# Kernel optimization log

Hardware: AMD Instinct MI355X
Metric: run time of the kernel (lower is better)

## Reference

```python
import jax, jax.numpy as jnp
import numpy as np

I = 16    # nutrition_input_size
H = 128   # hidden_size
B = 64
S = 4096
MLP = 64


def setup_inputs() -> dict:
    key = jax.random.key(0)
    ks = jax.random.split(key, 16)
    sc = 0.05
    inp = {
        "nutrition_data": jax.random.normal(ks[0], (B, S, I), dtype=jnp.float32),
        # GRU layer 0 (input size I)
        "w_ih0": sc * jax.random.normal(ks[1], (3 * H, I), dtype=jnp.float32),
        "w_hh0": sc * jax.random.normal(ks[2], (3 * H, H), dtype=jnp.float32),
        "b_ih0": sc * jax.random.normal(ks[3], (3 * H,), dtype=jnp.float32),
        "b_hh0": sc * jax.random.normal(ks[4], (3 * H,), dtype=jnp.float32),
        # GRU layer 1 (input size H)
        "w_ih1": sc * jax.random.normal(ks[5], (3 * H, H), dtype=jnp.float32),
        "w_hh1": sc * jax.random.normal(ks[6], (3 * H, H), dtype=jnp.float32),
        "b_ih1": sc * jax.random.normal(ks[7], (3 * H,), dtype=jnp.float32),
        "b_hh1": sc * jax.random.normal(ks[8], (3 * H,), dtype=jnp.float32),
        # metabolism increment head: Linear(H+I, 64) -> ReLU -> Linear(64, 1)
        "w1": sc * jax.random.normal(ks[9], (MLP, H + I), dtype=jnp.float32),
        "b1": sc * jax.random.normal(ks[10], (MLP,), dtype=jnp.float32),
        "w2": sc * jax.random.normal(ks[11], (1, MLP), dtype=jnp.float32),
        "b2": sc * jax.random.normal(ks[12], (1,), dtype=jnp.float32),
        "initial_metabolism": jnp.float32(2.5),
    }
    return inp


def _gru_layer(x, w_ih, w_hh, b_ih, b_hh):
    # x: [B, S, D]; PyTorch GRU cell math, gate order (r, z, n).
    gi = jnp.einsum("bsd,gd->bsg", x, w_ih) + b_ih  # [B, S, 3H]
    h0 = jnp.zeros((x.shape[0], w_hh.shape[1]), dtype=x.dtype)

    def step(h, gi_t):
        gh = h @ w_hh.T + b_hh  # [B, 3H]
        i_r, i_z, i_n = jnp.split(gi_t, 3, axis=-1)
        h_r, h_z, h_n = jnp.split(gh, 3, axis=-1)
        r = jax.nn.sigmoid(i_r + h_r)
        z = jax.nn.sigmoid(i_z + h_z)
        n = jnp.tanh(i_n + r * h_n)
        h_new = (1.0 - z) * n + z * h
        return h_new, h_new

    _, hs = jax.lax.scan(step, h0, jnp.swapaxes(gi, 0, 1))  # hs: [S, B, H]
    return jnp.swapaxes(hs, 0, 1)  # [B, S, H]


def reference(nutrition_data, w_ih0, w_hh0, b_ih0, b_hh0,
              w_ih1, w_hh1, b_ih1, b_hh1,
              w1, b1, w2, b2, initial_metabolism):
    # 2-layer GRU (dropout is inactive in eval; identical math without it)
    h1 = _gru_layer(nutrition_data, w_ih0, w_hh0, b_ih0, b_hh0)
    gru_out = _gru_layer(h1, w_ih1, w_hh1, b_ih1, b_hh1)  # [B, S, H]

    # Per-timestep head is independent of recurrence: batch it over all t,
    # then replace the sequential additive accumulation with a cumsum.
    combined = jnp.concatenate([gru_out, nutrition_data], axis=-1)  # [B, S, H+I]
    hdn = jax.nn.relu(jnp.einsum("bsf,mf->bsm", combined, w1) + b1)
    inc = jnp.tanh(jnp.einsum("bsm,om->bso", hdn, w2) + b2) * 0.125  # [B, S, 1]
    out = initial_metabolism + jnp.cumsum(inc, axis=1)  # [B, S, 1]
    return out
```

## Files before the change

kernel.cpp:

```cpp
#include <hip/hip_runtime.h>
#include <cmath>

#define B 64
#define S 4096
#define NI 16
#define H 128
#define F 144
#define CH 16
#define NCH (S / CH)
#define GIP 201

typedef _Float16 h2   __attribute__((ext_vector_type(2)));
typedef _Float16 h8   __attribute__((ext_vector_type(8)));
typedef float    f4v  __attribute__((ext_vector_type(4)));
typedef unsigned long long u64;
typedef u64 u64x2 __attribute__((ext_vector_type(2)));

__device__ __forceinline__ float rcp_fast(float x) { return __builtin_amdgcn_rcpf(x); }
__device__ __forceinline__ float sigf(float x) {
    return rcp_fast(1.0f + __expf(-x));
}
__device__ __forceinline__ float tanh_fast(float x) {
    const float e = __expf(-2.0f * x);
    return fmaf(2.0f, rcp_fast(1.0f + e), -1.0f);
}
__device__ __forceinline__ float pair_reduce(float v) {
    int t1 = __builtin_amdgcn_mov_dpp(__float_as_int(v), 0xB1, 0xf, 0xf, true);
    v += __int_as_float(t1);
    return v;
}
__device__ __forceinline__ h2 cvt2(float a, float b) {
    h2 r; r[0] = (_Float16)a; r[1] = (_Float16)b; return r;
}
__device__ __forceinline__ void cvt8(const float* p, h2* w) {
    const float4 f0 = ((const float4*)p)[0];
    const float4 f1 = ((const float4*)p)[1];
    w[0] = cvt2(f0.x, f0.y); w[1] = cvt2(f0.z, f0.w);
    w[2] = cvt2(f1.x, f1.y); w[3] = cvt2(f1.z, f1.w);
}
__device__ __forceinline__ h8 cvt8v(const float* p) {
    const float4 f0 = ((const float4*)p)[0];
    const float4 f1 = ((const float4*)p)[1];
    h8 r;
    r[0] = (_Float16)f0.x; r[1] = (_Float16)f0.y;
    r[2] = (_Float16)f0.z; r[3] = (_Float16)f0.w;
    r[4] = (_Float16)f1.x; r[5] = (_Float16)f1.y;
    r[6] = (_Float16)f1.z; r[7] = (_Float16)f1.w;
    return r;
}
__device__ __forceinline__ void pin_h2(h2& v) {
    int t = __builtin_bit_cast(int, v);
    asm volatile("" : "+v"(t));
    v = __builtin_bit_cast(h2, t);
}
__device__ __forceinline__ void pin_f(float& v) {
    asm volatile("" : "+v"(v));
}
__device__ __forceinline__ void pin_h8(h8& v) {
    u64x2 t = __builtin_bit_cast(u64x2, v);
    u64 a = t[0], b = t[1];
    asm volatile("" : "+v"(a), "+v"(b));
    t[0] = a; t[1] = b;
    v = __builtin_bit_cast(h8, t);
}
__device__ __forceinline__ f4v mfma16(h8 a, h8 b, f4v c) {
    return __builtin_amdgcn_mfma_f32_16x16x32_f16(a, b, c, 0, 0, 0);
}

__device__ __forceinline__ void store_y0(void* p, uint2 v) {
    __hip_atomic_store((u64*)p, __builtin_bit_cast(u64, v),
                       __ATOMIC_RELAXED, __HIP_MEMORY_SCOPE_AGENT);
}
__device__ __forceinline__ h8 load_y0_h8(const _Float16* p) {
    u64x2 v;
    v[0] = __hip_atomic_load((const u64*)p,     __ATOMIC_RELAXED, __HIP_MEMORY_SCOPE_AGENT);
    v[1] = __hip_atomic_load((const u64*)p + 1, __ATOMIC_RELAXED, __HIP_MEMORY_SCOPE_AGENT);
    return __builtin_bit_cast(h8, v);
}
__device__ __forceinline__ void wait_flag(int* f) {
    int spins = 0;
    while (__hip_atomic_load(f, __ATOMIC_ACQUIRE, __HIP_MEMORY_SCOPE_AGENT) == 0) {
        __builtin_amdgcn_s_sleep(8);
        if (++spins > (1 << 17)) break;
    }
}
__device__ __forceinline__ void post_flag(int* f) {
    __hip_atomic_store(f, 1, __ATOMIC_RELEASE, __HIP_MEMORY_SCOPE_AGENT);
}

__device__ __forceinline__ void write_gi(float* gp, const f4v* accs,
                                         const float* bias, int wv, int nl, int q) {
#pragma unroll
    for (int tt = 0; tt < 6; tt++) {
        const int n = 16 * (wv * 6 + tt) + nl;
        const int g = n >> 7, jj = n & 127;
#pragma unroll
        for (int r = 0; r < 4; r++)
            gp[((4 * q + r) * 3 + g) * GIP + jj] = accs[tt][r] + bias[tt];
    }
}

__global__ __launch_bounds__(512, 1)
void gru_pipe(const float* __restrict__ x,
              const float* __restrict__ w_ih0, const float* __restrict__ w_hh0,
              const float* __restrict__ b_ih0, const float* __restrict__ b_hh0,
              const float* __restrict__ w_ih1, const float* __restrict__ w_hh1,
              const float* __restrict__ b_ih1, const float* __restrict__ b_hh1,
              _Float16* __restrict__ hbuf, int* __restrict__ flags)
{
    __shared__ __align__(16) _Float16 sH[2][H];
    __shared__ __align__(16) float    sGi[2][CH][3][GIP];
    __shared__ __align__(16) _Float16 sO[2][CH][H];

    const int tid = threadIdx.x;
    const int b = blockIdx.x >> 1;
    const bool producer = (blockIdx.x & 1) == 0;
    const bool isRec = tid < 256;
    const int lane = tid & 63;
    const int jr = (tid & 255) >> 1;
    const int mr = tid & 1;
    const int wv = (tid >> 6) - 4;
    const int nl = lane & 15;
    const int q  = lane >> 4;

    const float* xb = x + (size_t)b * S * NI;
    _Float16*    yb = hbuf + (size_t)b * S * H;
    int*         fb = flags + b * NCH;

    h2 wc[96];
    float b_hn = 0.0f;
    h8 Bf[6][4];
    float bias[6];
    h8 Apre[4];

    if (isRec) {
        const float* whh = producer ? w_hh0 : w_hh1;
        const float* bhh = producer ? b_hh0 : b_hh1;
#pragma unroll
        for (int g = 0; g < 3; g++)
#pragma unroll
            for (int i = 0; i < 8; i++) {
                const int ii = (i + 4 * mr) & 7;
                cvt8(whh + (size_t)(g * H + jr) * H + 64 * mr + 8 * ii,
                     &wc[g * 32 + 4 * i]);
            }
        b_hn = bhh[2 * H + jr];
#pragma unroll
        for (int i = 0; i < 96; i++) pin_h2(wc[i]);
        pin_f(b_hn);
        if (tid < H) sH[0][tid] = (_Float16)0.0f;
    } else if (producer) {
#pragma unroll
        for (int tt = 0; tt < 6; tt++) {
            const int n = 16 * (wv * 6 + tt) + nl;
            if (q < 2) Bf[tt][0] = cvt8v(w_ih0 + (size_t)n * NI + 8 * q);
            else { h8 z = {}; Bf[tt][0] = z; }
            bias[tt] = b_ih0[n] + (n < 2 * H ? b_hh0[n] : 0.0f);
            pin_h8(Bf[tt][0]); pin_f(bias[tt]);
        }
        h8 A;
        if (q < 2) A = cvt8v(xb + (size_t)nl * NI + 8 * q);
        else { h8 z = {}; A = z; }
        f4v accs[6];
#pragma unroll
        for (int tt = 0; tt < 6; tt++) {
            f4v zz = {0.f, 0.f, 0.f, 0.f};
            accs[tt] = mfma16(A, Bf[tt][0], zz);
        }
        write_gi(&sGi[0][0][0][0], accs, bias, wv, nl, q);
    } else {
#pragma unroll
        for (int tt = 0; tt < 6; tt++) {
            const int n = 16 * (wv * 6 + tt) + nl;
            const float* wr = w_ih1 + (size_t)n * H;
#pragma unroll
            for (int kc = 0; kc < 4; kc++) {
                Bf[tt][kc] = cvt8v(wr + 32 * kc + 8 * q);
                pin_h8(Bf[tt][kc]);
            }
            bias[tt] = b_ih1[n] + (n < 2 * H ? b_hh1[n] : 0.0f);
            pin_f(bias[tt]);
        }
        if (lane == 0) wait_flag(fb + 0);
        const _Float16* yrow = yb + (size_t)nl * H;
        h8 A0c[4];
#pragma unroll
        for (int kc = 0; kc < 4; kc++)
            A0c[kc] = load_y0_h8(yrow + 32 * kc + 8 * q);
        f4v accs[6];
#pragma unroll
        for (int tt = 0; tt < 6; tt++) { f4v zz = {0.f,0.f,0.f,0.f}; accs[tt] = zz; }
#pragma unroll
        for (int kc = 0; kc < 4; kc++)
#pragma unroll
            for (int tt = 0; tt < 6; tt++)
                accs[tt] = mfma16(A0c[kc], Bf[tt][kc], accs[tt]);
        write_gi(&sGi[0][0][0][0], accs, bias, wv, nl, q);
    }
    float hprev = 0.0f;
    __syncthreads();

    for (int t = 0; t < S; t++) {
        const int cur = t & 1;
        const int c   = t >> 4;
        const int tw  = t & (CH - 1);

        if (isRec) {
            const float gr = sGi[c & 1][tw][0][jr];
            const float gz = sGi[c & 1][tw][1][jr];
            const float gn = sGi[c & 1][tw][2][jr];
            const float4* hv = (const float4*)&sH[cur][0];
            float ar = 0.f, az = 0.f, ahn = 0.f;
#pragma unroll
            for (int i = 0; i < 8; i++) {
                const int ii = (i + 4 * mr) & 7;
                const float4 qv = hv[8 * mr + ii];
                const h2 p0 = __builtin_bit_cast(h2, qv.x);
                const h2 p1 = __builtin_bit_cast(h2, qv.y);
                const h2 p2 = __builtin_bit_cast(h2, qv.z);
                const h2 p3 = __builtin_bit_cast(h2, qv.w);
                ar  = __builtin_amdgcn_fdot2(p0, wc[4*i+0],    ar,  false);
                ar  = __builtin_amdgcn_fdot2(p1, wc[4*i+1],    ar,  false);
                ar  = __builtin_amdgcn_fdot2(p2, wc[4*i+2],    ar,  false);
                ar  = __builtin_amdgcn_fdot2(p3, wc[4*i+3],    ar,  false);
                az  = __builtin_amdgcn_fdot2(p0, wc[32+4*i+0], az,  false);
                az  = __builtin_amdgcn_fdot2(p1, wc[32+4*i+1], az,  false);
                az  = __builtin_amdgcn_fdot2(p2, wc[32+4*i+2], az,  false);
                az  = __builtin_amdgcn_fdot2(p3, wc[32+4*i+3], az,  false);
                ahn = __builtin_amdgcn_fdot2(p0, wc[64+4*i+0], ahn, false);
                ahn = __builtin_amdgcn_fdot2(p1, wc[64+4*i+1], ahn, false);
                ahn = __builtin_amdgcn_fdot2(p2, wc[64+4*i+2], ahn, false);
                ahn = __builtin_amdgcn_fdot2(p3, wc[64+4*i+3], ahn, false);
            }
            const float r  = sigf(pair_reduce(ar) + gr);
            const float z  = sigf(pair_reduce(az) + gz);
            const float n  = tanh_fast(gn + r * (pair_reduce(ahn) + b_hn));
            const float hn = n + z * (hprev - n);
            hprev = hn;
            if (mr == 0) {
                sH[cur ^ 1][jr]   = (_Float16)hn;
                sO[c & 1][tw][jr] = (_Float16)hn;
            }
        } else {
            if (tw == 0) {
                if (c >= 1) {
                    const int cp  = c - 1;
                    const int idx = tid - 256;
                    const uint2 v0 = ((const uint2*)&sO[cp & 1][0][0])[idx];
                    const uint2 v1 = ((const uint2*)&sO[cp & 1][0][0])[idx + 256];
                    if (producer) {
                        store_y0((char*)(yb + (size_t)cp * CH * H) + 8 * idx, v0);
                        store_y0((char*)(yb + (size_t)cp * CH * H) + 8 * (idx + 256), v1);
                    } else {
                        ((uint2*)(yb + (size_t)cp * CH * H))[idx]       = v0;
                        ((uint2*)(yb + (size_t)cp * CH * H))[idx + 256] = v1;
                    }
                }
                if (c + 1 < NCH) {
                    if (producer) {
                        if (q < 2) Apre[0] = cvt8v(xb + ((size_t)(c + 1) * CH + nl) * NI + 8 * q);
                        else { h8 z = {}; Apre[0] = z; }
                    } else {
                        if (lane == 0) wait_flag(fb + (c + 1));
                        const _Float16* yr2 = yb + ((size_t)(c + 1) * CH + nl) * H;
#pragma unroll
                        for (int kc = 0; kc < 4; kc++)
                            Apre[kc] = load_y0_h8(yr2 + 32 * kc + 8 * q);
                    }
                }
            } else if (tw == 1) {
                if (producer && c >= 1 && tid == 256) post_flag(fb + (c - 1));
                if (c + 1 < NCH) {
                    f4v accs[6];
#pragma unroll
                    for (int tt = 0; tt < 6; tt++) { f4v zz = {0.f,0.f,0.f,0.f}; accs[tt] = zz; }
                    if (producer) {
#pragma unroll
                        for (int tt = 0; tt < 6; tt++)
                            accs[tt] = mfma16(Apre[0], Bf[tt][0], accs[tt]);
                    } else {
#pragma unroll
                        for (int kc = 0; kc < 4; kc++)
#pragma unroll
                            for (int tt = 0; tt < 6; tt++)
                                accs[tt] = mfma16(Apre[kc], Bf[tt][kc], accs[tt]);
                    }
                    write_gi(&sGi[(c + 1) & 1][0][0][0], accs, bias, wv, nl, q);
                }
            }
        }
        __syncthreads();
    }
    if (!isRec) {
        const int cp  = NCH - 1;
        const int idx = tid - 256;
        const uint2 v0 = ((const uint2*)&sO[cp & 1][0][0])[idx];
        const uint2 v1 = ((const uint2*)&sO[cp & 1][0][0])[idx + 256];
        if (producer) {
            store_y0((char*)(yb + (size_t)cp * CH * H) + 8 * idx, v0);
            store_y0((char*)(yb + (size_t)cp * CH * H) + 8 * (idx + 256), v1);
        } else {
            ((uint2*)(yb + (size_t)cp * CH * H))[idx]       = v0;
            ((uint2*)(yb + (size_t)cp * CH * H))[idx + 256] = v1;
        }
    }
    __syncthreads();
    if (producer && tid == 256) post_flag(fb + (NCH - 1));
}

__global__ __launch_bounds__(256, 2)
void head_mfma(const _Float16* __restrict__ h1, const float* __restrict__ x,
               const float* __restrict__ w1, const float* __restrict__ b1,
               const float* __restrict__ w2, const float* __restrict__ b2,
               float* __restrict__ inc)
{
    const int wave = threadIdx.x >> 6;
    const int lane = threadIdx.x & 63;
    const int nl   = lane & 15;
    const int q    = lane >> 4;

    h8 Bf[4][5];
    float b1v[4], w2v[4];
#pragma unroll
    for (int t = 0; t < 4; t++) {
        const int n = 16 * t + nl;
        const float* wr = w1 + (size_t)n * F;
#pragma unroll
        for (int c = 0; c < 4; c++)
            Bf[t][c] = cvt8v(wr + 32 * c + 8 * q);
        if (q < 2) Bf[t][4] = cvt8v(wr + 128 + 8 * q);
        else { h8 z = {};
               Bf[t][4] = z; }
        b1v[t] = b1[n];
        w2v[t] = w2[n];
    }
    const float b2v = b2[0];

    const int gw = blockIdx.x * 4 + wave;

    for (int it = 0; it < 8; it++) {
        const int row0 = (gw * 8 + it) * 16;
        const int rm   = row0 + nl;

        const _Float16* hp = h1 + (size_t)rm * H;
        h8 A0 = *(const h8*)(hp + 8 * q);
        h8 A1 = *(const h8*)(hp + 32 + 8 * q);
        h8 A2 = *(const h8*)(hp + 64 + 8 * q);
        h8 A3 = *(const h8*)(hp + 96 + 8 * q);
        h8 A4;
        if (q < 2) A4 = cvt8v(x + (size_t)rm * NI + 8 * q);
        else { h8 z = {}; A4 = z; }

        f4v acc0 = {0.f,0.f,0.f,0.f}, acc1 = {0.f,0.f,0.f,0.f};
        f4v acc2 = {0.f,0.f,0.f,0.f}, acc3 = {0.f,0.f,0.f,0.f};
        acc0 = mfma16(A0, Bf[0][0], acc0); acc1 = mfma16(A0, Bf[1][0], acc1);
        acc2 = mfma16(A0, Bf[2][0], acc2); acc3 = mfma16(A0, Bf[3][0], acc3);
        acc0 = mfma16(A1, Bf[0][1], acc0); acc1 = mfma16(A1, Bf[1][1], acc1);
        acc2 = mfma16(A1, Bf[2][1], acc2); acc3 = mfma16(A1, Bf[3][1], acc3);
        acc0 = mfma16(A2, Bf[0][2], acc0); acc1 = mfma16(A2, Bf[1][2], acc1);
        acc2 = mfma16(A2, Bf[2][2], acc2); acc3 = mfma16(A2, Bf[3][2], acc3);
// ... 39 lines not shown

    const float* ib = inc + (size_t)b * S;
    float v[16];
#pragma unroll
    for (int i = 0; i < 16; i++) v[i] = ib[tid * 16 + i];

    float run = 0.f;
#pragma unroll
    for (int i = 0; i < 16; i++) { run += v[i]; v[i] = run; }

    float t = run;
#pragma unroll
    for (int off = 1; off < 64; off <<= 1) {
        float u = __shfl_up(t, off, 64);
        if (lane >= off) t += u;
    }
    const float excl = t - run;
    if (lane == 63) sW[wid] = t;
    __syncthreads();

    float wo = 0.f;
#pragma unroll
    for (int w = 0; w < 4; w++) if (w < wid) wo += sW[w];

    const float prefix = wo + excl + init[0];
    float* ob = out + (size_t)b * S;
#pragma unroll
    for (int i = 0; i < 16; i++) ob[tid * 16 + i] = prefix + v[i];
}

extern "C" void kernel_launch(void* const* d_in, const int* in_sizes, int n_in,
                              void* d_out, int out_size, void* d_ws, size_t ws_size,
                              hipStream_t stream)
{
    (void)in_sizes; (void)n_in; (void)out_size; (void)ws_size;
    const float* x     = (const float*)d_in[0];
    const float* w_ih0 = (const float*)d_in[1];
    const float* w_hh0 = (const float*)d_in[2];
    const float* b_ih0 = (const float*)d_in[3];
    const float* b_hh0 = (const float*)d_in[4];
    const float* w_ih1 = (const float*)d_in[5];
    const float* w_hh1 = (const float*)d_in[6];
    const float* b_ih1 = (const float*)d_in[7];
    const float* b_hh1 = (const float*)d_in[8];
    const float* w1    = (const float*)d_in[9];
    const float* b1    = (const float*)d_in[10];
    const float* w2    = (const float*)d_in[11];
    const float* b2    = (const float*)d_in[12];
    const float* init  = (const float*)d_in[13];
    float* out = (float*)d_out;

    _Float16* hbuf = (_Float16*)d_ws;
    float* incbuf  = (float*)((char*)d_ws + (size_t)B * S * H * 2);
    int* flags     = (int*)((char*)d_ws + (size_t)B * S * H * 2
                                        + (size_t)B * S * 4);

    hipMemsetAsync(flags, 0, (size_t)B * NCH * sizeof(int), stream);

    hipLaunchKernelGGL(gru_pipe, dim3(2 * B), dim3(512), 0, stream,
                       x, w_ih0, w_hh0, b_ih0, b_hh0,
                       w_ih1, w_hh1, b_ih1, b_hh1, hbuf, flags);
    hipLaunchKernelGGL(head_mfma, dim3(512), dim3(256), 0, stream,
                       hbuf, x, w1, b1, w2, b2, incbuf);
    hipLaunchKernelGGL(cumsum_kernel, dim3(B), dim3(256), 0, stream,
                       incbuf, init, out);
}
```

Before: 3.078 ms.

## Fuse both GRU layers into one block per batch with LDS handoff

Replaces the producer/consumer block pairs, which passed layer-0 outputs through global memory guarded by atomic flags, with a single 768-thread block per batch row. Wave groups run the layer-0 recurrence (input projection folded in via fdot2 on x staged in LDS), the layer-1 recurrence, and an MFMA group that computes layer-1 input gates from layer-0 outputs held in LDS and writes the final hidden states. This removes global round trips, flag spinning and the memset launch. In exchange it uses half as many blocks (64 CUs), adds a two-chunk pipeline skew, and makes all three roles share one barrier every step.

```diff
diff --git a/kernel.cpp b/kernel.cpp
--- a/kernel.cpp
+++ b/kernel.cpp
@@ -8,9 +8,10 @@
 #define F 144
 #define CH 16
 #define NCH (S / CH)
-#define GIP 201
+#define GIP 132
 
 typedef _Float16 h2   __attribute__((ext_vector_type(2)));
+typedef _Float16 h4v  __attribute__((ext_vector_type(4)));
 typedef _Float16 h8   __attribute__((ext_vector_type(8)));
 typedef float    f4v  __attribute__((ext_vector_type(4)));
 typedef unsigned long long u64;
@@ -67,75 +68,44 @@
     return __builtin_amdgcn_mfma_f32_16x16x32_f16(a, b, c, 0, 0, 0);
 }
 
-__device__ __forceinline__ void store_y0(void* p, uint2 v) {
-    __hip_atomic_store((u64*)p, __builtin_bit_cast(u64, v),
-                       __ATOMIC_RELAXED, __HIP_MEMORY_SCOPE_AGENT);
-}
-__device__ __forceinline__ h8 load_y0_h8(const _Float16* p) {
-    u64x2 v;
-    v[0] = __hip_atomic_load((const u64*)p,     __ATOMIC_RELAXED, __HIP_MEMORY_SCOPE_AGENT);
-    v[1] = __hip_atomic_load((const u64*)p + 1, __ATOMIC_RELAXED, __HIP_MEMORY_SCOPE_AGENT);
-    return __builtin_bit_cast(h8, v);
-}
-__device__ __forceinline__ void wait_flag(int* f) {
-    int spins = 0;
-    while (__hip_atomic_load(f, __ATOMIC_ACQUIRE, __HIP_MEMORY_SCOPE_AGENT) == 0) {
-        __builtin_amdgcn_s_sleep(8);
-        if (++spins > (1 << 17)) break;
-    }
-}
-__device__ __forceinline__ void post_flag(int* f) {
-    __hip_atomic_store(f, 1, __ATOMIC_RELEASE, __HIP_MEMORY_SCOPE_AGENT);
-}
-
-__device__ __forceinline__ void write_gi(float* gp, const f4v* accs,
-                                         const float* bias, int wv, int nl, int q) {
-#pragma unroll
-    for (int tt = 0; tt < 6; tt++) {
-        const int n = 16 * (wv * 6 + tt) + nl;
-        const int g = n >> 7, jj = n & 127;
-#pragma unroll
-        for (int r = 0; r < 4; r++)
-            gp[((4 * q + r) * 3 + g) * GIP + jj] = accs[tt][r] + bias[tt];
-    }
-}
-
-__global__ __launch_bounds__(512, 1)
-void gru_pipe(const float* __restrict__ x,
-              const float* __restrict__ w_ih0, const float* __restrict__ w_hh0,
-              const float* __restrict__ b_ih0, const float* __restrict__ b_hh0,
-              const float* __restrict__ w_ih1, const float* __restrict__ w_hh1,
-              const float* __restrict__ b_ih1, const float* __restrict__ b_hh1,
-              _Float16* __restrict__ hbuf, int* __restrict__ flags)
+__global__ __launch_bounds__(768, 1)
+void gru_fused(const float* __restrict__ x,
+               const float* __restrict__ w_ih0, const float* __restrict__ w_hh0,
+               const float* __restrict__ b_ih0, const float* __restrict__ b_hh0,
+               const float* __restrict__ w_ih1, const float* __restrict__ w_hh1,
+               const float* __restrict__ b_ih1, const float* __restrict__ b_hh1,
+               _Float16* __restrict__ h_out)
 {
-    __shared__ __align__(16) _Float16 sH[2][H];
+    __shared__ __align__(16) _Float16 sH0[2][H];
+    __shared__ __align__(16) _Float16 sH1[2][H];
+    __shared__ __align__(16) _Float16 sX[2][CH][NI];
+    __shared__ __align__(16) _Float16 sY[2][CH][H];
+    __shared__ __align__(16) _Float16 sHo[2][CH][H];
     __shared__ __align__(16) float    sGi[2][CH][3][GIP];
-    __shared__ __align__(16) _Float16 sO[2][CH][H];
-
-    const int tid = threadIdx.x;
-    const int b = blockIdx.x >> 1;
-    const bool producer = (blockIdx.x & 1) == 0;
-    const bool isRec = tid < 256;
+
+    const int tid  = threadIdx.x;
+    const int b    = blockIdx.x;
+    const int wave = tid >> 6;
     const int lane = tid & 63;
-    const int jr = (tid & 255) >> 1;
-    const int mr = tid & 1;
-    const int wv = (tid >> 6) - 4;
-    const int nl = lane & 15;
-    const int q  = lane >> 4;
+    const int role = wave >> 2;
+    const int rt   = tid & 255;
+    const int jr   = rt >> 1;
+    const int mr   = rt & 1;
+    const int wv   = wave & 3;
+    const int nl   = lane & 15;
+    const int q    = lane >> 4;
 
     const float* xb = x + (size_t)b * S * NI;
-    _Float16*    yb = hbuf + (size_t)b * S * H;
-    int*         fb = flags + b * NCH;
+    _Float16*    hb = h_out + (size_t)b * S * H;
 
     h2 wc[96];
-    float b_hn = 0.0f;
+    h2 wx[12];
+    float b_r = 0.f, b_z = 0.f, b_in = 0.f, b_hn = 0.f;
     h8 Bf[6][4];
     float bias[6];
-    h8 Apre[4];
-
-    if (isRec) {
-        const float* whh = producer ? w_hh0 : w_hh1;
-        const float* bhh = producer ? b_hh0 : b_hh1;
+
+    if (role < 2) {
+        const float* whh = role == 0 ? w_hh0 : w_hh1;
 #pragma unroll
         for (int g = 0; g < 3; g++)
 #pragma unroll
@@ -144,30 +114,25 @@
                 cvt8(whh + (size_t)(g * H + jr) * H + 64 * mr + 8 * ii,
                      &wc[g * 32 + 4 * i]);
             }
-        b_hn = bhh[2 * H + jr];
 #pragma unroll
         for (int i = 0; i < 96; i++) pin_h2(wc[i]);
+        if (role == 0) {
+#pragma unroll
+            for (int g = 0; g < 3; g++)
+                cvt8(w_ih0 + (size_t)(g * H + jr) * NI + 8 * mr, &wx[g * 4]);
+#pragma unroll
+            for (int i = 0; i < 12; i++) pin_h2(wx[i]);
+            b_r  = b_ih0[jr]       + b_hh0[jr];
+            b_z  = b_ih0[H + jr]   + b_hh0[H + jr];
+            b_in = b_ih0[2*H + jr];
+            b_hn = b_hh0[2*H + jr];
+            pin_f(b_r); pin_f(b_z); pin_f(b_in);
+            if (rt < H) sH0[0][rt] = (_Float16)0.0f;
+        } else {
+            b_hn = b_hh1[2*H + jr];
+            if (rt < H) sH1[0][rt] = (_Float16)0.0f;
+        }
         pin_f(b_hn);
-        if (tid < H) sH[0][tid] = (_Float16)0.0f;
-    } else if (producer) {
-#pragma unroll
-        for (int tt = 0; tt < 6; tt++) {
-            const int n = 16 * (wv * 6 + tt) + nl;
-            if (q < 2) Bf[tt][0] = cvt8v(w_ih0 + (size_t)n * NI + 8 * q);
-            else { h8 z = {}; Bf[tt][0] = z; }
-            bias[tt] = b_ih0[n] + (n < 2 * H ? b_hh0[n] : 0.0f);
-            pin_h8(Bf[tt][0]); pin_f(bias[tt]);
-        }
-        h8 A;
-        if (q < 2) A = cvt8v(xb + (size_t)nl * NI + 8 * q);
-        else { h8 z = {}; A = z; }
-        f4v accs[6];
-#pragma unroll
-        for (int tt = 0; tt < 6; tt++) {
-            f4v zz = {0.f, 0.f, 0.f, 0.f};
-            accs[tt] = mfma16(A, Bf[tt][0], zz);
-        }
-        write_gi(&sGi[0][0][0][0], accs, bias, wv, nl, q);
     } else {
 #pragma unroll
         for (int tt = 0; tt < 6; tt++) {
@@ -181,131 +146,175 @@
             bias[tt] = b_ih1[n] + (n < 2 * H ? b_hh1[n] : 0.0f);
             pin_f(bias[tt]);
         }
-        if (lane == 0) wait_flag(fb + 0);
-        const _Float16* yrow = yb + (size_t)nl * H;
-        h8 A0c[4];
-#pragma unroll
-        for (int kc = 0; kc < 4; kc++)
-            A0c[kc] = load_y0_h8(yrow + 32 * kc + 8 * q);
-        f4v accs[6];
-#pragma unroll
-        for (int tt = 0; tt < 6; tt++) { f4v zz = {0.f,0.f,0.f,0.f}; accs[tt] = zz; }
-#pragma unroll
-        for (int kc = 0; kc < 4; kc++)
-#pragma unroll
-            for (int tt = 0; tt < 6; tt++)
-                accs[tt] = mfma16(A0c[kc], Bf[tt][kc], accs[tt]);
-        write_gi(&sGi[0][0][0][0], accs, bias, wv, nl, q);
+    }
+
+    float4 xreg = {0.f, 0.f, 0.f, 0.f};
+    if (tid < 64) {
+        const float4 v = ((const float4*)xb)[tid];
+        h4v p; p[0] = (_Float16)v.x; p[1] = (_Float16)v.y;
+               p[2] = (_Float16)v.z; p[3] = (_Float16)v.w;
+        ((h4v*)&sX[0][0][0])[tid] = p;
+        xreg = ((const float4*)(xb + CH * NI))[tid];
     }
     float hprev = 0.0f;
     __syncthreads();
 
-    for (int t = 0; t < S; t++) {
+    for (int t = 0; t < S + 2 * CH; t++) {
         const int cur = t & 1;
         const int c   = t >> 4;
         const int tw  = t & (CH - 1);
 
-        if (isRec) {
-            const float gr = sGi[c & 1][tw][0][jr];
-            const float gz = sGi[c & 1][tw][1][jr];
-            const float gn = sGi[c & 1][tw][2][jr];
-            const float4* hv = (const float4*)&sH[cur][0];
-            float ar = 0.f, az = 0.f, ahn = 0.f;
-#pragma unroll
-            for (int i = 0; i < 8; i++) {
-                const int ii = (i + 4 * mr) & 7;
-                const float4 qv = hv[8 * mr + ii];
-                const h2 p0 = __builtin_bit_cast(h2, qv.x);
-                const h2 p1 = __builtin_bit_cast(h2, qv.y);
-                const h2 p2 = __builtin_bit_cast(h2, qv.z);
-                const h2 p3 = __builtin_bit_cast(h2, qv.w);
-                ar  = __builtin_amdgcn_fdot2(p0, wc[4*i+0],    ar,  false);
-                ar  = __builtin_amdgcn_fdot2(p1, wc[4*i+1],    ar,  false);
-                ar  = __builtin_amdgcn_fdot2(p2, wc[4*i+2],    ar,  false);
-                ar  = __builtin_amdgcn_fdot2(p3, wc[4*i+3],    ar,  false);
-                az  = __builtin_amdgcn_fdot2(p0, wc[32+4*i+0], az,  false);
-                az  = __builtin_amdgcn_fdot2(p1, wc[32+4*i+1], az,  false);
-                az  = __builtin_amdgcn_fdot2(p2, wc[32+4*i+2], az,  false);
-                az  = __builtin_amdgcn_fdot2(p3, wc[32+4*i+3], az,  false);
-                ahn = __builtin_amdgcn_fdot2(p0, wc[64+4*i+0], ahn, false);
-                ahn = __builtin_amdgcn_fdot2(p1, wc[64+4*i+1], ahn, false);
-                ahn = __builtin_amdgcn_fdot2(p2, wc[64+4*i+2], ahn, false);
-                ahn = __builtin_amdgcn_fdot2(p3, wc[64+4*i+3], ahn, false);
+        if (role == 0) {
+            if (t < S) {
+                if (tw == 0 && tid < 64) {
+                    const int cn = c + 1;
+                    if (cn < NCH) {
+                        h4v p; p[0] = (_Float16)xreg.x; p[1] = (_Float16)xreg.y;
+                               p[2] = (_Float16)xreg.z; p[3] = (_Float16)xreg.w;
+                        ((h4v*)&sX[cn & 1][0][0])[tid] = p;
+                        if (cn + 1 < NCH)
+                            xreg = ((const float4*)(xb + (size_t)(cn + 1) * CH * NI))[tid];
+                    }
+                }
+                const float4* hv = (const float4*)&sH0[cur][0];
+                float ar = 0.f, az = 0.f, ahn = 0.f;
+#pragma unroll
+                for (int i = 0; i < 8; i++) {
+                    const int ii = (i + 4 * mr) & 7;
+                    const float4 qv = hv[8 * mr + ii];
+                    const h2 p0 = __builtin_bit_cast(h2, qv.x);
+                    const h2 p1 = __builtin_bit_cast(h2, qv.y);
+                    const h2 p2 = __builtin_bit_cast(h2, qv.z);
+                    const h2 p3 = __builtin_bit_cast(h2, qv.w);
+                    ar  = __builtin_amdgcn_fdot2(p0, wc[4*i+0],    ar,  false);
+                    ar  = __builtin_amdgcn_fdot2(p1, wc[4*i+1],    ar,  false);
+                    ar  = __builtin_amdgcn_fdot2(p2, wc[4*i+2],    ar,  false);
+                    ar  = __builtin_amdgcn_fdot2(p3, wc[4*i+3],    ar,  false);
+                    az  = __builtin_amdgcn_fdot2(p0, wc[32+4*i+0], az,  false);
+                    az  = __builtin_amdgcn_fdot2(p1, wc[32+4*i+1], az,  false);
+                    az  = __builtin_amdgcn_fdot2(p2, wc[32+4*i+2], az,  false);
+                    az  = __builtin_amdgcn_fdot2(p3, wc[32+4*i+3], az,  false);
+                    ahn = __builtin_amdgcn_fdot2(p0, wc[64+4*i+0], ahn, false);
+                    ahn = __builtin_amdgcn_fdot2(p1, wc[64+4*i+1], ahn, false);
+                    ahn = __builtin_amdgcn_fdot2(p2, wc[64+4*i+2], ahn, false);
+                    ahn = __builtin_amdgcn_fdot2(p3, wc[64+4*i+3], ahn, false);
+                }
+                const float4 xq = *(const float4*)&sX[c & 1][tw][8 * mr];
+                const h2 x0 = __builtin_bit_cast(h2, xq.x);
+                const h2 x1 = __builtin_bit_cast(h2, xq.y);
+                const h2 x2 = __builtin_bit_cast(h2, xq.z);
+                const h2 x3 = __builtin_bit_cast(h2, xq.w);
+                float ain = 0.f;
+                ar  = __builtin_amdgcn_fdot2(x0, wx[0],  ar,  false);
+                ar  = __builtin_amdgcn_fdot2(x1, wx[1],  ar,  false);
+                ar  = __builtin_amdgcn_fdot2(x2, wx[2],  ar,  false);
+                ar  = __builtin_amdgcn_fdot2(x3, wx[3],  ar,  false);
+                az  = __builtin_amdgcn_fdot2(x0, wx[4],  az,  false);
+                az  = __builtin_amdgcn_fdot2(x1, wx[5],  az,  false);
+                az  = __builtin_amdgcn_fdot2(x2, wx[6],  az,  false);
+                az  = __builtin_amdgcn_fdot2(x3, wx[7],  az,  false);
+                ain = __builtin_amdgcn_fdot2(x0, wx[8],  ain, false);
+                ain = __builtin_amdgcn_fdot2(x1, wx[9],  ain, false);
+                ain = __builtin_amdgcn_fdot2(x2, wx[10], ain, false);
+                ain = __builtin_amdgcn_fdot2(x3, wx[11], ain, false);
+
+                const float r  = sigf(pair_reduce(ar) + b_r);
+                const float z  = sigf(pair_reduce(az) + b_z);
+                const float n  = tanh_fast(pair_reduce(ain) + b_in
+                                           + r * (pair_reduce(ahn) + b_hn));
+                const float hn = n + z * (hprev - n);
+                hprev = hn;
+                if (mr == 0) {
+                    sH0[cur ^ 1][jr]  = (_Float16)hn;
+                    sY[c & 1][tw][jr] = (_Float16)hn;
+                }
             }
-            const float r  = sigf(pair_reduce(ar) + gr);
-            const float z  = sigf(pair_reduce(az) + gz);
-            const float n  = tanh_fast(gn + r * (pair_reduce(ahn) + b_hn));
-            const float hn = n + z * (hprev - n);
-            hprev = hn;
-            if (mr == 0) {
-                sH[cur ^ 1][jr]   = (_Float16)hn;
-                sO[c & 1][tw][jr] = (_Float16)hn;
+        } else if (role == 1) {
+            if (t >= 2 * CH) {
+                const float gr = sGi[c & 1][tw][0][jr];
+                const float gz = sGi[c & 1][tw][1][jr];
+                const float gn = sGi[c & 1][tw][2][jr];
+                const float4* hv = (const float4*)&sH1[cur][0];
+                float ar = 0.f, az = 0.f, ahn = 0.f;
+#pragma unroll
+                for (int i = 0; i < 8; i++) {
+                    const int ii = (i + 4 * mr) & 7;
+                    const float4 qv = hv[8 * mr + ii];
+                    const h2 p0 = __builtin_bit_cast(h2, qv.x);
+                    const h2 p1 = __builtin_bit_cast(h2, qv.y);
+                    const h2 p2 = __builtin_bit_cast(h2, qv.z);
+                    const h2 p3 = __builtin_bit_cast(h2, qv.w);
+                    ar  = __builtin_amdgcn_fdot2(p0, wc[4*i+0],    ar,  false);
+                    ar  = __builtin_amdgcn_fdot2(p1, wc[4*i+1],    ar,  false);
+                    ar  = __builtin_amdgcn_fdot2(p2, wc[4*i+2],    ar,  false);
+                    ar  = __builtin_amdgcn_fdot2(p3, wc[4*i+3],    ar,  false);
+                    az  = __builtin_amdgcn_fdot2(p0, wc[32+4*i+0], az,  false);
+                    az  = __builtin_amdgcn_fdot2(p1, wc[32+4*i+1], az,  false);
+                    az  = __builtin_amdgcn_fdot2(p2, wc[32+4*i+2], az,  false);
+                    az  = __builtin_amdgcn_fdot2(p3, wc[32+4*i+3], az,  false);
+                    ahn = __builtin_amdgcn_fdot2(p0, wc[64+4*i+0], ahn, false);
+                    ahn = __builtin_amdgcn_fdot2(p1, wc[64+4*i+1], ahn, false);
+                    ahn = __builtin_amdgcn_fdot2(p2, wc[64+4*i+2], ahn, false);
+                    ahn = __builtin_amdgcn_fdot2(p3, wc[64+4*i+3], ahn, false);
+                }
+                const float r  = sigf(pair_reduce(ar) + gr);
+                const float z  = sigf(pair_reduce(az) + gz);
+                const float n  = tanh_fast(gn + r * (pair_reduce(ahn) + b_hn));
+                const float hn = n + z * (hprev - n);
+                hprev = hn;
+                if (mr == 0) {
+                    sH1[cur ^ 1][jr]   = (_Float16)hn;
+                    sHo[c & 1][tw][jr] = (_Float16)hn;
+                }
             }
         } else {
             if (tw == 0) {
-                if (c >= 1) {
-                    const int cp  = c - 1;
-                    const int idx = tid - 256;
-                    const uint2 v0 = ((const uint2*)&sO[cp & 1][0][0])[idx];
-                    const uint2 v1 = ((const uint2*)&sO[cp & 1][0][0])[idx + 256];
-                    if (producer) {
-                        store_y0((char*)(yb + (size_t)cp * CH * H) + 8 * idx, v0);
-                        store_y0((char*)(yb + (size_t)cp * CH * H) + 8 * (idx + 256), v1);
-                    } else {
-                        ((uint2*)(yb + (size_t)cp * CH * H))[idx]       = v0;
-                        ((uint2*)(yb + (size_t)cp * CH * H))[idx + 256] = v1;
+                if (c >= 3) {
+                    const int k   = c - 3;
+                    const int idx = tid - 512;
+                    const uint2 v0 = ((const uint2*)&sHo[k & 1][0][0])[idx];
+                    const uint2 v1 = ((const uint2*)&sHo[k & 1][0][0])[idx + 256];
+                    ((uint2*)(hb + (size_t)k * CH * H))[idx]       = v0;
+                    ((uint2*)(hb + (size_t)k * CH * H))[idx + 256] = v1;
+                }
+            } else if (tw == 1) {
+                if (c >= 1 && c <= NCH) {
+                    const int k = c - 1;
+                    const _Float16* yr = &sY[k & 1][nl][0];
+                    h8 A[4];
+#pragma unroll
+                    for (int kc = 0; kc < 4; kc++)
+                        A[kc] = *(const h8*)(yr + 32 * kc + 8 * q);
+                    f4v accs[6];
+#pragma unroll
+                    for (int tt = 0; tt < 6; tt++) { f4v zz = {0.f,0.f,0.f,0.f}; accs[tt] = zz; }
+#pragma unroll
+                    for (int kc = 0; kc < 4; kc++)
+#pragma unroll
+                        for (int tt = 0; tt < 6; tt++)
+                            accs[tt] = mfma16(A[kc], Bf[tt][kc], accs[tt]);
+                    float* gp = &sGi[k & 1][0][0][0];
+#pragma unroll
+                    for (int tt = 0; tt < 6; tt++) {
+                        const int n = 16 * (wv * 6 + tt) + nl;
+                        const int g = n >> 7, jj = n & 127;
+#pragma unroll
+                        for (int r = 0; r < 4; r++)
+                            gp[((4 * q + r) * 3 + g) * GIP + jj] = accs[tt][r] + bias[tt];
                     }
                 }
-                if (c + 1 < NCH) {
-                    if (producer) {
-                        if (q < 2) Apre[0] = cvt8v(xb + ((size_t)(c + 1) * CH + nl) * NI + 8 * q);
-                        else { h8 z = {}; Apre[0] = z; }
-                    } else {
-                        if (lane == 0) wait_flag(fb + (c + 1));
-                        const _Float16* yr2 = yb + ((size_t)(c + 1) * CH + nl) * H;
-#pragma unroll
-                        for (int kc = 0; kc < 4; kc++)
-                            Apre[kc] = load_y0_h8(yr2 + 32 * kc + 8 * q);
-                    }
-                }
-            } else if (tw == 1) {
-                if (producer && c >= 1 && tid == 256) post_flag(fb + (c - 1));
-                if (c + 1 < NCH) {
-                    f4v accs[6];
-#pragma unroll
-                    for (int tt = 0; tt < 6; tt++) { f4v zz = {0.f,0.f,0.f,0.f}; accs[tt] = zz; }
-                    if (producer) {
-#pragma unroll
-                        for (int tt = 0; tt < 6; tt++)
-                            accs[tt] = mfma16(Apre[0], Bf[tt][0], accs[tt]);
-                    } else {
-#pragma unroll
-                        for (int kc = 0; kc < 4; kc++)
-#pragma unroll
-                            for (int tt = 0; tt < 6; tt++)
-                                accs[tt] = mfma16(Apre[kc], Bf[tt][kc], accs[tt]);
-                    }
-                    write_gi(&sGi[(c + 1) & 1][0][0][0], accs, bias, wv, nl, q);
-                }
             }
         }
         __syncthreads();
     }
-    if (!isRec) {
-        const int cp  = NCH - 1;
-        const int idx = tid - 256;
-        const uint2 v0 = ((const uint2*)&sO[cp & 1][0][0])[idx];
-        const uint2 v1 = ((const uint2*)&sO[cp & 1][0][0])[idx + 256];
-        if (producer) {
-            store_y0((char*)(yb + (size_t)cp * CH * H) + 8 * idx, v0);
-            store_y0((char*)(yb + (size_t)cp * CH * H) + 8 * (idx + 256), v1);
-        } else {
-            ((uint2*)(yb + (size_t)cp * CH * H))[idx]       = v0;
-            ((uint2*)(yb + (size_t)cp * CH * H))[idx + 256] = v1;
-        }
-    }
-    __syncthreads();
-    if (producer && tid == 256) post_flag(fb + (NCH - 1));
+    if (role == 2) {
+        const int k   = NCH - 1;
+        const int idx = tid - 512;
+        const uint2 v0 = ((const uint2*)&sHo[k & 1][0][0])[idx];
+        const uint2 v1 = ((const uint2*)&sHo[k & 1][0][0])[idx + 256];
+        ((uint2*)(hb + (size_t)k * CH * H))[idx]       = v0;
+        ((uint2*)(hb + (size_t)k * CH * H))[idx + 256] = v1;
+    }
 }
 
 __global__ __launch_bounds__(256, 2)
@@ -451,14 +460,10 @@
 
     _Float16* hbuf = (_Float16*)d_ws;
     float* incbuf  = (float*)((char*)d_ws + (size_t)B * S * H * 2);
-    int* flags     = (int*)((char*)d_ws + (size_t)B * S * H * 2
-                                        + (size_t)B * S * 4);
-
-    hipMemsetAsync(flags, 0, (size_t)B * NCH * sizeof(int), stream);
-
-    hipLaunchKernelGGL(gru_pipe, dim3(2 * B), dim3(512), 0, stream,
+
+    hipLaunchKernelGGL(gru_fused, dim3(B), dim3(768), 0, stream,
                        x, w_ih0, w_hh0, b_ih0, b_hh0,
-                       w_ih1, w_hh1, b_ih1, b_hh1, hbuf, flags);
+                       w_ih1, w_hh1, b_ih1, b_hh1, hbuf);
     hipLaunchKernelGGL(head_mfma, dim3(512), dim3(256), 0, stream,
                        hbuf, x, w1, b1, w2, b2, incbuf);
     hipLaunchKernelGGL(cumsum_kernel, dim3(B), dim3(256), 0, stream,
```

After: 4.228 ms. 1.37x slower.

## Replace block-wide barriers with LDS flag polling between recurrence and input-projection waves

Applied to the files above, without the earlier changes.

Shrinks the GRU block from 512 to 256 threads. Two waves now run the recurrence, each thread owning one hidden unit with all 384 half-precision weight pairs in registers, so the DPP pair reduction goes away. Two more waves compute the input projection and flush hidden states to global memory. The per-timestep __syncthreads is replaced by counters in shared memory that each side polls, so the projection waves run ahead on their own schedule and the recurrence waves only handshake with each other. The costs are heavy register pressure, spin-wait overhead on every step, and a risk of stalls if the polling ordering is wrong.

```diff
diff --git a/kernel.cpp b/kernel.cpp
--- a/kernel.cpp
+++ b/kernel.cpp
@@ -8,7 +8,7 @@
 #define F 144
 #define CH 16
 #define NCH (S / CH)
-#define GIP 201
+#define GIP 129
 
 typedef _Float16 h2   __attribute__((ext_vector_type(2)));
 typedef _Float16 h8   __attribute__((ext_vector_type(8)));
@@ -23,11 +23,6 @@
 __device__ __forceinline__ float tanh_fast(float x) {
     const float e = __expf(-2.0f * x);
     return fmaf(2.0f, rcp_fast(1.0f + e), -1.0f);
-}
-__device__ __forceinline__ float pair_reduce(float v) {
-    int t1 = __builtin_amdgcn_mov_dpp(__float_as_int(v), 0xB1, 0xf, 0xf, true);
-    v += __int_as_float(t1);
-    return v;
 }
 __device__ __forceinline__ h2 cvt2(float a, float b) {
     h2 r; r[0] = (_Float16)a; r[1] = (_Float16)b; return r;
@@ -53,9 +48,7 @@
     asm volatile("" : "+v"(t));
     v = __builtin_bit_cast(h2, t);
 }
-__device__ __forceinline__ void pin_f(float& v) {
-    asm volatile("" : "+v"(v));
-}
+__device__ __forceinline__ void pin_f(float& v) { asm volatile("" : "+v"(v)); }
 __device__ __forceinline__ void pin_h8(h8& v) {
     u64x2 t = __builtin_bit_cast(u64x2, v);
     u64 a = t[0], b = t[1];
@@ -67,6 +60,17 @@
     return __builtin_amdgcn_mfma_f32_16x16x32_f16(a, b, c, 0, 0, 0);
 }
 
+__device__ __forceinline__ void poll_ge(int* p, int v) {
+    int spins = 0;
+    while (__hip_atomic_load(p, __ATOMIC_ACQUIRE, __HIP_MEMORY_SCOPE_WORKGROUP) < v) {
+        __builtin_amdgcn_s_sleep(1);
+        if (++spins > (1 << 20)) break;
+    }
+}
+__device__ __forceinline__ void publish(int* p, int v) {
+    __hip_atomic_store(p, v, __ATOMIC_RELEASE, __HIP_MEMORY_SCOPE_WORKGROUP);
+}
+
 __device__ __forceinline__ void store_y0(void* p, uint2 v) {
     __hip_atomic_store((u64*)p, __builtin_bit_cast(u64, v),
                        __ATOMIC_RELAXED, __HIP_MEMORY_SCOPE_AGENT);
@@ -88,20 +92,8 @@
     __hip_atomic_store(f, 1, __ATOMIC_RELEASE, __HIP_MEMORY_SCOPE_AGENT);
 }
 
-__device__ __forceinline__ void write_gi(float* gp, const f4v* accs,
-                                         const float* bias, int wv, int nl, int q) {
-#pragma unroll
-    for (int tt = 0; tt < 6; tt++) {
-        const int n = 16 * (wv * 6 + tt) + nl;
-        const int g = n >> 7, jj = n & 127;
-#pragma unroll
-        for (int r = 0; r < 4; r++)
-            gp[((4 * q + r) * 3 + g) * GIP + jj] = accs[tt][r] + bias[tt];
-    }
-}
-
-__global__ __launch_bounds__(512, 1)
-void gru_pipe(const float* __restrict__ x,
+__global__ __launch_bounds__(256, 1)
+void gru_poll(const float* __restrict__ x,
               const float* __restrict__ w_ih0, const float* __restrict__ w_hh0,
               const float* __restrict__ b_ih0, const float* __restrict__ b_hh0,
               const float* __restrict__ w_ih1, const float* __restrict__ w_hh1,
@@ -111,201 +103,223 @@
     __shared__ __align__(16) _Float16 sH[2][H];
     __shared__ __align__(16) float    sGi[2][CH][3][GIP];
     __shared__ __align__(16) _Float16 sO[2][CH][H];
-
-    const int tid = threadIdx.x;
-    const int b = blockIdx.x >> 1;
+    __shared__ int sCnt[2];
+    __shared__ int sGiDone[2];
+    __shared__ int sFlush[2];
+
+    const int tid  = threadIdx.x;
+    const int wave = tid >> 6;
+    const int lane = tid & 63;
+    const int b    = blockIdx.x >> 1;
     const bool producer = (blockIdx.x & 1) == 0;
-    const bool isRec = tid < 256;
-    const int lane = tid & 63;
-    const int jr = (tid & 255) >> 1;
-    const int mr = tid & 1;
-    const int wv = (tid >> 6) - 4;
-    const int nl = lane & 15;
-    const int q  = lane >> 4;
-
-    const float* xb = x + (size_t)b * S * NI;
-    _Float16*    yb = hbuf + (size_t)b * S * H;
-    int*         fb = flags + b * NCH;
-
-    h2 wc[96];
-    float b_hn = 0.0f;
-    h8 Bf[6][4];
-    float bias[6];
-    h8 Apre[4];
-
-    if (isRec) {
-        const float* whh = producer ? w_hh0 : w_hh1;
-        const float* bhh = producer ? b_hh0 : b_hh1;
+
+    _Float16* yb = hbuf + (size_t)b * S * H;
+    int*      fb = flags + b * NCH;
+
+    if (tid == 0) {
+        sCnt[0] = 0; sCnt[1] = 0;
+        sGiDone[0] = 0; sGiDone[1] = 0;
+        sFlush[0] = 0; sFlush[1] = 0;
+    }
+    __syncthreads();
+
+    if (wave < 2) {
+        const int j = 64 * wave + lane;
+        const float* Whh = producer ? w_hh0 : w_hh1;
+        const float* Bhh = producer ? b_hh0 : b_hh1;
+
+        h2 w[192];
 #pragma unroll
         for (int g = 0; g < 3; g++)
 #pragma unroll
+            for (int i = 0; i < 16; i++)
+                cvt8(Whh + (size_t)(g * H + j) * H + 8 * i, &w[g * 64 + 4 * i]);
+        float b_hn = Bhh[2 * H + j];
+#pragma unroll
+        for (int i = 0; i < 192; i++) pin_h2(w[i]);
+        pin_f(b_hn);
+
+        float4 hv[16];
+#pragma unroll
+        for (int i = 0; i < 16; i++) hv[i] = make_float4(0.f, 0.f, 0.f, 0.f);
+        float hprev = 0.0f;
+
+        int* me = &sCnt[wave];
+        int* ot = &sCnt[wave ^ 1];
+
+        for (int t = 0; t < S; t++) {
+            const int c = t >> 4, tw = t & 15;
+            if (tw == 0) {
+                poll_ge(&sGiDone[0], c + 1);
+                poll_ge(&sGiDone[1], c + 1);
+            }
+            const float gr = sGi[c & 1][tw][0][j];
+            const float gz = sGi[c & 1][tw][1][j];
+            const float gn = sGi[c & 1][tw][2][j];
+
+            float ar0 = 0.f, az0 = 0.f, an0 = 0.f;
+            float ar1 = 0.f, az1 = 0.f, an1 = 0.f;
+#pragma unroll
             for (int i = 0; i < 8; i++) {
-                const int ii = (i + 4 * mr) & 7;
-                cvt8(whh + (size_t)(g * H + jr) * H + 64 * mr + 8 * ii,
-                     &wc[g * 32 + 4 * i]);
-            }
-        b_hn = bhh[2 * H + jr];
-#pragma unroll
-        for (int i = 0; i < 96; i++) pin_h2(wc[i]);
-        pin_f(b_hn);
-        if (tid < H) sH[0][tid] = (_Float16)0.0f;
-    } else if (producer) {
-#pragma unroll
-        for (int tt = 0; tt < 6; tt++) {
-            const int n = 16 * (wv * 6 + tt) + nl;
-            if (q < 2) Bf[tt][0] = cvt8v(w_ih0 + (size_t)n * NI + 8 * q);
-            else { h8 z = {}; Bf[tt][0] = z; }
-            bias[tt] = b_ih0[n] + (n < 2 * H ? b_hh0[n] : 0.0f);
-            pin_h8(Bf[tt][0]); pin_f(bias[tt]);
-        }
-        h8 A;
-        if (q < 2) A = cvt8v(xb + (size_t)nl * NI + 8 * q);
-        else { h8 z = {}; A = z; }
-        f4v accs[6];
-#pragma unroll
-        for (int tt = 0; tt < 6; tt++) {
-            f4v zz = {0.f, 0.f, 0.f, 0.f};
-            accs[tt] = mfma16(A, Bf[tt][0], zz);
-        }
-        write_gi(&sGi[0][0][0][0], accs, bias, wv, nl, q);
-    } else {
-#pragma unroll
-        for (int tt = 0; tt < 6; tt++) {
-            const int n = 16 * (wv * 6 + tt) + nl;
-            const float* wr = w_ih1 + (size_t)n * H;
-#pragma unroll
-            for (int kc = 0; kc < 4; kc++) {
-                Bf[tt][kc] = cvt8v(wr + 32 * kc + 8 * q);
-                pin_h8(Bf[tt][kc]);
-            }
-            bias[tt] = b_ih1[n] + (n < 2 * H ? b_hh1[n] : 0.0f);
-            pin_f(bias[tt]);
-        }
-        if (lane == 0) wait_flag(fb + 0);
-        const _Float16* yrow = yb + (size_t)nl * H;
-        h8 A0c[4];
-#pragma unroll
-        for (int kc = 0; kc < 4; kc++)
-            A0c[kc] = load_y0_h8(yrow + 32 * kc + 8 * q);
-        f4v accs[6];
-#pragma unroll
-        for (int tt = 0; tt < 6; tt++) { f4v zz = {0.f,0.f,0.f,0.f}; accs[tt] = zz; }
-#pragma unroll
-        for (int kc = 0; kc < 4; kc++)
-#pragma unroll
-            for (int tt = 0; tt < 6; tt++)
-                accs[tt] = mfma16(A0c[kc], Bf[tt][kc], accs[tt]);
-        write_gi(&sGi[0][0][0][0], accs, bias, wv, nl, q);
-    }
-    float hprev = 0.0f;
-    __syncthreads();
-
-    for (int t = 0; t < S; t++) {
-        const int cur = t & 1;
-        const int c   = t >> 4;
-        const int tw  = t & (CH - 1);
-
-        if (isRec) {
-            const float gr = sGi[c & 1][tw][0][jr];
-            const float gz = sGi[c & 1][tw][1][jr];
-            const float gn = sGi[c & 1][tw][2][jr];
-            const float4* hv = (const float4*)&sH[cur][0];
-            float ar = 0.f, az = 0.f, ahn = 0.f;
-#pragma unroll
-            for (int i = 0; i < 8; i++) {
-                const int ii = (i + 4 * mr) & 7;
-                const float4 qv = hv[8 * mr + ii];
-                const h2 p0 = __builtin_bit_cast(h2, qv.x);
-                const h2 p1 = __builtin_bit_cast(h2, qv.y);
-                const h2 p2 = __builtin_bit_cast(h2, qv.z);
-                const h2 p3 = __builtin_bit_cast(h2, qv.w);
-                ar  = __builtin_amdgcn_fdot2(p0, wc[4*i+0],    ar,  false);
-                ar  = __builtin_amdgcn_fdot2(p1, wc[4*i+1],    ar,  false);
-                ar  = __builtin_amdgcn_fdot2(p2, wc[4*i+2],    ar,  false);
-                ar  = __builtin_amdgcn_fdot2(p3, wc[4*i+3],    ar,  false);
-                az  = __builtin_amdgcn_fdot2(p0, wc[32+4*i+0], az,  false);
-                az  = __builtin_amdgcn_fdot2(p1, wc[32+4*i+1], az,  false);
-                az  = __builtin_amdgcn_fdot2(p2, wc[32+4*i+2], az,  false);
-                az  = __builtin_amdgcn_fdot2(p3, wc[32+4*i+3], az,  false);
-                ahn = __builtin_amdgcn_fdot2(p0, wc[64+4*i+0], ahn, false);
-                ahn = __builtin_amdgcn_fdot2(p1, wc[64+4*i+1], ahn, false);
-                ahn = __builtin_amdgcn_fdot2(p2, wc[64+4*i+2], ahn, false);
-                ahn = __builtin_amdgcn_fdot2(p3, wc[64+4*i+3], ahn, false);
-            }
-            const float r  = sigf(pair_reduce(ar) + gr);
-            const float z  = sigf(pair_reduce(az) + gz);
-            const float n  = tanh_fast(gn + r * (pair_reduce(ahn) + b_hn));
+                const float4 q = hv[i];
+                const h2 p0 = __builtin_bit_cast(h2, q.x);
+                const h2 p1 = __builtin_bit_cast(h2, q.y);
+                const h2 p2 = __builtin_bit_cast(h2, q.z);
+                const h2 p3 = __builtin_bit_cast(h2, q.w);
+                ar0 = __builtin_amdgcn_fdot2(p0, w[4*i+0],     ar0, false);
+                ar0 = __builtin_amdgcn_fdot2(p1, w[4*i+1],     ar0, false);
+                ar0 = __builtin_amdgcn_fdot2(p2, w[4*i+2],     ar0, false);
+                ar0 = __builtin_amdgcn_fdot2(p3, w[4*i+3],     ar0, false);
+                az0 = __builtin_amdgcn_fdot2(p0, w[64+4*i+0],  az0, false);
+                az0 = __builtin_amdgcn_fdot2(p1, w[64+4*i+1],  az0, false);
+                az0 = __builtin_amdgcn_fdot2(p2, w[64+4*i+2],  az0, false);
+                az0 = __builtin_amdgcn_fdot2(p3, w[64+4*i+3],  az0, false);
+                an0 = __builtin_amdgcn_fdot2(p0, w[128+4*i+0], an0, false);
+                an0 = __builtin_amdgcn_fdot2(p1, w[128+4*i+1], an0, false);
+                an0 = __builtin_amdgcn_fdot2(p2, w[128+4*i+2], an0, false);
+                an0 = __builtin_amdgcn_fdot2(p3, w[128+4*i+3], an0, false);
+            }
+#pragma unroll
+            for (int i = 8; i < 16; i++) {
+                const float4 q = hv[i];
+                const h2 p0 = __builtin_bit_cast(h2, q.x);
+                const h2 p1 = __builtin_bit_cast(h2, q.y);
+                const h2 p2 = __builtin_bit_cast(h2, q.z);
+                const h2 p3 = __builtin_bit_cast(h2, q.w);
+                ar1 = __builtin_amdgcn_fdot2(p0, w[4*i+0],     ar1, false);
+                ar1 = __builtin_amdgcn_fdot2(p1, w[4*i+1],     ar1, false);
+                ar1 = __builtin_amdgcn_fdot2(p2, w[4*i+2],     ar1, false);
+                ar1 = __builtin_amdgcn_fdot2(p3, w[4*i+3],     ar1, false);
+                az1 = __builtin_amdgcn_fdot2(p0, w[64+4*i+0],  az1, false);
+                az1 = __builtin_amdgcn_fdot2(p1, w[64+4*i+1],  az1, false);
+                az1 = __builtin_amdgcn_fdot2(p2, w[64+4*i+2],  az1, false);
+                az1 = __builtin_amdgcn_fdot2(p3, w[64+4*i+3],  az1, false);
+                an1 = __builtin_amdgcn_fdot2(p0, w[128+4*i+0], an1, false);
+                an1 = __builtin_amdgcn_fdot2(p1, w[128+4*i+1], an1, false);
+                an1 = __builtin_amdgcn_fdot2(p2, w[128+4*i+2], an1, false);
+                an1 = __builtin_amdgcn_fdot2(p3, w[128+4*i+3], an1, false);
+            }
+            const float r  = sigf(ar0 + ar1 + gr);
+            const float z  = sigf(az0 + az1 + gz);
+            const float n  = tanh_fast(gn + r * (an0 + an1 + b_hn));
             const float hn = n + z * (hprev - n);
             hprev = hn;
-            if (mr == 0) {
-                sH[cur ^ 1][jr]   = (_Float16)hn;
-                sO[c & 1][tw][jr] = (_Float16)hn;
-            }
-        } else {
-            if (tw == 0) {
-                if (c >= 1) {
-                    const int cp  = c - 1;
-                    const int idx = tid - 256;
-                    const uint2 v0 = ((const uint2*)&sO[cp & 1][0][0])[idx];
-                    const uint2 v1 = ((const uint2*)&sO[cp & 1][0][0])[idx + 256];
-                    if (producer) {
-                        store_y0((char*)(yb + (size_t)cp * CH * H) + 8 * idx, v0);
-                        store_y0((char*)(yb + (size_t)cp * CH * H) + 8 * (idx + 256), v1);
-                    } else {
-                        ((uint2*)(yb + (size_t)cp * CH * H))[idx]       = v0;
-                        ((uint2*)(yb + (size_t)cp * CH * H))[idx + 256] = v1;
+
+            sH[t & 1][j]     = (_Float16)hn;
+            sO[c & 1][tw][j] = (_Float16)hn;
+            publish(me, t + 1);
+            poll_ge(ot, t + 1);
+            const float4* hb = (const float4*)&sH[t & 1][0];
+#pragma unroll
+            for (int i = 0; i < 16; i++) hv[i] = hb[i];
+        }
+    } else {
+        const int hw = wave - 2;
+        const int nl = lane & 15;
+        const int q  = lane >> 4;
+        const float* xb = x + (size_t)b * S * NI;
+
+        h8 Bf4[12][4];
+        h8 Bf1[12];
+        float bias[12];
+#pragma unroll
+        for (int tt = 0; tt < 12; tt++) {
+            const int n = 16 * (hw * 12 + tt) + nl;
+            if (producer) {
+                if (q < 2) Bf1[tt] = cvt8v(w_ih0 + (size_t)n * NI + 8 * q);
+                else { h8 zz = {}; Bf1[tt] = zz; }
+                pin_h8(Bf1[tt]);
+                bias[tt] = b_ih0[n] + (n < 2 * H ? b_hh0[n] : 0.0f);
+            } else {
+                const float* wr = w_ih1 + (size_t)n * H;
+#pragma unroll
+                for (int kc = 0; kc < 4; kc++) {
+                    Bf4[tt][kc] = cvt8v(wr + 32 * kc + 8 * q);
+                    pin_h8(Bf4[tt][kc]);
+                }
+                bias[tt] = b_ih1[n] + (n < 2 * H ? b_hh1[n] : 0.0f);
+            }
+            pin_f(bias[tt]);
+        }
+
+        for (int c = 0; c < NCH; c++) {
+            if (c >= 2) {
+                poll_ge(&sCnt[0], 16 * (c - 1));
+                poll_ge(&sCnt[1], 16 * (c - 1));
+                const int k = c - 2;
+                const uint2* src = (const uint2*)&sO[c & 1][0][0];
+#pragma unroll
+                for (int e = 0; e < 4; e++) {
+                    const int idx = hw * 256 + 64 * e + lane;
+                    const uint2 v = src[idx];
+                    if (producer)
+                        store_y0((char*)(yb + (size_t)k * CH * H) + 8 * idx, v);
+                    else
+                        *(uint2*)((char*)(yb + (size_t)k * CH * H) + 8 * idx) = v;
+                }
+                if (producer) {
+                    publish(&sFlush[hw], c - 1);
+                    if (hw == 0) {
+                        poll_ge(&sFlush[1], c - 1);
+                        if (lane == 0) post_flag(fb + k);
                     }
                 }
-                if (c + 1 < NCH) {
-                    if (producer) {
-                        if (q < 2) Apre[0] = cvt8v(xb + ((size_t)(c + 1) * CH + nl) * NI + 8 * q);
-                        else { h8 z = {}; Apre[0] = z; }
-                    } else {
-                        if (lane == 0) wait_flag(fb + (c + 1));
-                        const _Float16* yr2 = yb + ((size_t)(c + 1) * CH + nl) * H;
-#pragma unroll
-                        for (int kc = 0; kc < 4; kc++)
-                            Apre[kc] = load_y0_h8(yr2 + 32 * kc + 8 * q);
-                    }
+            }
+            f4v accs[12];
+#pragma unroll
+            for (int tt = 0; tt < 12; tt++) { f4v zz = {0.f,0.f,0.f,0.f}; accs[tt] = zz; }
+            if (producer) {
+                h8 A;
+                if (q < 2) A = cvt8v(xb + (size_t)(16 * c + nl) * NI + 8 * q);
+                else { h8 zz = {}; A = zz; }
+#pragma unroll
+                for (int tt = 0; tt < 12; tt++) accs[tt] = mfma16(A, Bf1[tt], accs[tt]);
+            } else {
+                if (lane == 0) wait_flag(fb + c);
+                const _Float16* yr = yb + (size_t)(16 * c + nl) * H;
+                h8 A[4];
+#pragma unroll
+                for (int kc = 0; kc < 4; kc++)
+                    A[kc] = load_y0_h8(yr + 32 * kc + 8 * q);
+#pragma unroll
+                for (int kc = 0; kc < 4; kc++)
+#pragma unroll
+                    for (int tt = 0; tt < 12; tt++)
+                        accs[tt] = mfma16(A[kc], Bf4[tt][kc], accs[tt]);
+            }
+            float* gp = &sGi[c & 1][0][0][0];
+#pragma unroll
+            for (int tt = 0; tt < 12; tt++) {
+                const int n = 16 * (hw * 12 + tt) + nl;
+                const int g = n >> 7, jj = n & 127;
+#pragma unroll
+                for (int r = 0; r < 4; r++)
+                    gp[((4 * q + r) * 3 + g) * GIP + jj] = accs[tt][r] + bias[tt];
+            }
+            publish(&sGiDone[hw], c + 1);
+        }
+        for (int k = NCH - 2; k < NCH; k++) {
+            poll_ge(&sCnt[0], 16 * (k + 1));
+            poll_ge(&sCnt[1], 16 * (k + 1));
+            const uint2* src = (const uint2*)&sO[k & 1][0][0];
+#pragma unroll
+            for (int e = 0; e < 4; e++) {
+                const int idx = hw * 256 + 64 * e + lane;
+                const uint2 v = src[idx];
+                if (producer)
+                    store_y0((char*)(yb + (size_t)k * CH * H) + 8 * idx, v);
+                else
+                    *(uint2*)((char*)(yb + (size_t)k * CH * H) + 8 * idx) = v;
+            }
+            if (producer) {
+                publish(&sFlush[hw], k + 1);
+                if (hw == 0) {
+                    poll_ge(&sFlush[1], k + 1);
+                    if (lane == 0) post_flag(fb + k);
                 }
-            } else if (tw == 1) {
-                if (producer && c >= 1 && tid == 256) post_flag(fb + (c - 1));
-                if (c + 1 < NCH) {
-                    f4v accs[6];
-#pragma unroll
-                    for (int tt = 0; tt < 6; tt++) { f4v zz = {0.f,0.f,0.f,0.f}; accs[tt] = zz; }
-                    if (producer) {
-#pragma unroll
-                        for (int tt = 0; tt < 6; tt++)
-                            accs[tt] = mfma16(Apre[0], Bf[tt][0], accs[tt]);
-                    } else {
-#pragma unroll
-                        for (int kc = 0; kc < 4; kc++)
-#pragma unroll
-                            for (int tt = 0; tt < 6; tt++)
-                                accs[tt] = mfma16(Apre[kc], Bf[tt][kc], accs[tt]);
-                    }
-                    write_gi(&sGi[(c + 1) & 1][0][0][0], accs, bias, wv, nl, q);
-                }
-            }
-        }
-        __syncthreads();
-    }
-    if (!isRec) {
-        const int cp  = NCH - 1;
-        const int idx = tid - 256;
-        const uint2 v0 = ((const uint2*)&sO[cp & 1][0][0])[idx];
-        const uint2 v1 = ((const uint2*)&sO[cp & 1][0][0])[idx + 256];
-        if (producer) {
-            store_y0((char*)(yb + (size_t)cp * CH * H) + 8 * idx, v0);
-            store_y0((char*)(yb + (size_t)cp * CH * H) + 8 * (idx + 256), v1);
-        } else {
-            ((uint2*)(yb + (size_t)cp * CH * H))[idx]       = v0;
-            ((uint2*)(yb + (size_t)cp * CH * H))[idx + 256] = v1;
-        }
-    }
-    __syncthreads();
-    if (producer && tid == 256) post_flag(fb + (NCH - 1));
+            }
+        }
+    }
 }
 
 __global__ __launch_bounds__(256, 2)
@@ -456,7 +470,7 @@
 
     hipMemsetAsync(flags, 0, (size_t)B * NCH * sizeof(int), stream);
 
-    hipLaunchKernelGGL(gru_pipe, dim3(2 * B), dim3(512), 0, stream,
+    hipLaunchKernelGGL(gru_poll, dim3(2 * B), dim3(256), 0, stream,
                        x, w_ih0, w_hh0, b_ih0, b_hh0,
                        w_ih1, w_hh1, b_ih1, b_hh1, hbuf, flags);
     hipLaunchKernelGGL(head_mfma, dim3(512), dim3(256), 0, stream,
```

New measurement: 2.868 ms. 6.8% less time.
